# Kernel optimization log

Measured on AMD Instinct MI355X. Metric: run time of the kernel, lower is better.

The kernel has to match this reference:

```python
import jax, jax.numpy as jnp
import numpy as np

B, INSIZE, H, OUT, STEPS = 8192, 256, 128, 1, 50


def setup_inputs() -> dict:
    key = jax.random.key(0)
    ks = jax.random.split(key, 16)
    s = 0.05
    inp = {
        "x": jax.random.normal(ks[0], (B, INSIZE), jnp.float32),
        # encoder MLP: 256 -> 128 -> 128 -> 128 (ReLU on hiddens, linear out)
        "ew0": jax.random.normal(ks[1], (INSIZE, 128), jnp.float32) * s,
        "eb0": jnp.zeros((128,), jnp.float32),
        "ew1": jax.random.normal(ks[2], (128, 128), jnp.float32) * s,
        "eb1": jnp.zeros((128,), jnp.float32),
        "ew2": jax.random.normal(ks[3], (128, H), jnp.float32) * s,
        "eb2": jnp.zeros((H,), jnp.float32),
        # GRU (input size OUT=1, hidden H=128), PyTorch layout [3H, in]/[3H, H]
        "w_ih": jax.random.normal(ks[4], (3 * H, OUT), jnp.float32) * s,
        "w_hh": jax.random.normal(ks[5], (3 * H, H), jnp.float32) * s,
        "b_ih": jnp.zeros((3 * H,), jnp.float32),
        "b_hh": jnp.zeros((3 * H,), jnp.float32),
        # decoder MLP: 128 -> 16 -> 1
        "dw0": jax.random.normal(ks[6], (H, 16), jnp.float32) * s,
        "db0": jnp.zeros((16,), jnp.float32),
        "dw1": jax.random.normal(ks[7], (16, OUT), jnp.float32) * s,
        "db1": jnp.zeros((OUT,), jnp.float32),
    }
    return inp


def _gru_cell(x_t, h, w_ih, w_hh, b_ih, b_hh):
    # PyTorch GRU cell: gates ordered [r, z, n]
    gx = x_t @ w_ih.T + b_ih  # [B, 3H]
    gh = h @ w_hh.T + b_hh    # [B, 3H]
    r = jax.nn.sigmoid(gx[:, :H] + gh[:, :H])
    z = jax.nn.sigmoid(gx[:, H:2 * H] + gh[:, H:2 * H])
    n = jnp.tanh(gx[:, 2 * H:] + r * gh[:, 2 * H:])
    return (1.0 - z) * n + z * h


def reference(x, ew0, eb0, ew1, eb1, ew2, eb2, w_ih, w_hh, b_ih, b_hh, dw0, db0, dw1, db1):
    # encoder MLP -> initial hidden state
    h = jax.nn.relu(x @ ew0 + eb0)
    h = jax.nn.relu(h @ ew1 + eb1)
    h = h @ ew2 + eb2  # [B, H]

    def step(carry, _):
        prev, hc = carry
        hn = _gru_cell(prev, hc, w_ih, w_hh, b_ih, b_hh)
        d = jax.nn.relu(hn @ dw0 + db0)
        out = d @ dw1 + db1  # [B, 1]
        return (out, hn), out

    prev0 = jnp.zeros((x.shape[0], OUT), x.dtype)
    _, outs = jax.lax.scan(step, (prev0, h), None, length=STEPS)  # [50, B, 1]
    outs = jnp.squeeze(outs, -1).T  # [B, 50]
    # torch: cat([zeros, out_0..out_49], dim=1)[..., :-1] -> [zeros, out_0..out_48]
    zeros = jnp.zeros((x.shape[0], 1), x.dtype)
    return jnp.concatenate([zeros, outs], axis=1)[:, :-1]
```

## Files before the change

### kernel.cpp

```cpp
#include <hip/hip_runtime.h>

#define NTH 256

typedef _Float16 half8 __attribute__((ext_vector_type(8)));
typedef _Float16 half4 __attribute__((ext_vector_type(4)));
typedef __attribute__((ext_vector_type(4))) float floatx4;

#define LOG2E 1.44269504088896340736f

template<int CTRL>
__device__ __forceinline__ float dpp_add(float v) {
    int o = __builtin_amdgcn_update_dpp(0, __float_as_int(v), CTRL, 0xF, 0xF, true);
    return v + __int_as_float(o);
}

#define MFMA16 __builtin_amdgcn_mfma_f32_16x16x32_f16

template<int KTILES, int CMASK, int ROWH>
__device__ __forceinline__ void enc_layer(const _Float16* __restrict__ src,
                                          const float* __restrict__ W,
                                          const float* __restrict__ bias,
                                          int w, int quad, int l15,
                                          floatx4 acc[2]) {
    half8 bw[2][KTILES];
    #pragma unroll
    for (int nt = 0; nt < 2; nt++) {
        const int jc = w * 32 + nt * 16 + l15;
        #pragma unroll
        for (int kt = 0; kt < KTILES; kt++) {
            const int kb = kt * 32 + quad * 8;
            half8 hv;
            #pragma unroll
            for (int e = 0; e < 8; e++) hv[e] = (_Float16)W[(kb + e) * 128 + jc];
            bw[nt][kt] = hv;
        }
        const float bv = bias[jc];
        acc[nt] = (floatx4){bv, bv, bv, bv};
    }
    #pragma unroll
    for (int kt = 0; kt < KTILES; kt++) {
        const half8 av = *(const half8*)(src + l15 * ROWH +
                                         (((kt * 4 + quad) + l15) & CMASK) * 8);
        acc[0] = MFMA16(av, bw[0][kt], acc[0], 0, 0, 0);
        acc[1] = MFMA16(av, bw[1][kt], acc[1], 0, 0, 0);
    }
}

__device__ __forceinline__ void enc_store(_Float16* __restrict__ dst,
                                          const floatx4 acc[2],
                                          int w, int quad, int l15, bool relu) {
    #pragma unroll
    for (int nt = 0; nt < 2; nt++) {
        const int jc = w * 32 + nt * 16 + l15;
        #pragma unroll
        for (int reg = 0; reg < 4; reg++) {
            const int row = quad * 4 + reg;
            float v = acc[nt][reg];
            if (relu) v = fmaxf(v, 0.f);
            dst[row * 128 + ((((jc >> 3) + row) & 15) << 3) + (jc & 7)] = (_Float16)v;
        }
    }
}

__global__ __launch_bounds__(NTH, 2)
void gru_fused_kernel(const float* __restrict__ x,
                      const float* __restrict__ ew0, const float* __restrict__ eb0,
                      const float* __restrict__ ew1, const float* __restrict__ eb1,
                      const float* __restrict__ ew2, const float* __restrict__ eb2,
                      const float* __restrict__ w_ih, const float* __restrict__ w_hh,
                      const float* __restrict__ b_ih, const float* __restrict__ b_hh,
                      const float* __restrict__ dw0, const float* __restrict__ db0,
                      const float* __restrict__ dw1, const float* __restrict__ db1,
                      float* __restrict__ out) {
    __shared__ __align__(16) _Float16 encx[16 * 256];
    __shared__ __align__(16) _Float16 h1b[16 * 128];
    __shared__ __align__(16) _Float16 h16[2 * 16 * 128];
    __shared__ float outb[16][52];

    const int tid  = threadIdx.x;
    const int b0   = blockIdx.x * 16;
    const int lane = tid & 63;
    const int w    = tid >> 6;
    const int quad = lane >> 4;
    const int l15  = lane & 15;

    #pragma unroll
    for (int i = 0; i < 4; i++) {
        const int e = tid + i * NTH;
        const int row = e >> 6, c4 = e & 63;
        const float4 xv = *(const float4*)(x + (size_t)(b0 + row) * 256 + c4 * 4);
        half4 hv = {(_Float16)xv.x, (_Float16)xv.y, (_Float16)xv.z, (_Float16)xv.w};
        *(half4*)(encx + row * 256 + (((c4 >> 1) + row) & 31) * 8 + (c4 & 1) * 4) = hv;
    }
    __syncthreads();

    floatx4 ea[2];
    enc_layer<8, 31, 256>(encx, ew0, eb0, w, quad, l15, ea);
    enc_store(h1b, ea, w, quad, l15, true);
    __syncthreads();
    enc_layer<4, 15, 128>(h1b, ew1, eb1, w, quad, l15, ea);
    enc_store(encx, ea, w, quad, l15, true);
    __syncthreads();
    enc_layer<4, 15, 128>(encx, ew2, eb2, w, quad, l15, ea);
    float hold[2][4];
    #pragma unroll
    for (int nt = 0; nt < 2; nt++)
        #pragma unroll
        for (int reg = 0; reg < 4; reg++) hold[nt][reg] = ea[nt][reg];
    enc_store(h16, ea, w, quad, l15, false);
    if (tid < 16) outb[tid][0] = 0.f;

    half8 wb16[3][2][4];
    #pragma unroll
    for (int g = 0; g < 3; g++) {
        const float scale = (g == 2) ? 2.f * LOG2E : LOG2E;
        #pragma unroll
        for (int nt = 0; nt < 2; nt++) {
            const float* wrow = w_hh + (g * 128 + w * 32 + nt * 16 + l15) * 128;
            #pragma unroll
            for (int kt = 0; kt < 4; kt++) {
                const int kb = kt * 32 + quad * 8;
                half8 hv;
                #pragma unroll
                for (int e = 0; e < 8; e++) hv[e] = (_Float16)(wrow[kb + e] * scale);
                wb16[g][nt][kt] = hv;
            }
        }
    }
    half8 dw16[4];
    #pragma unroll
    for (int kt = 0; kt < 4; kt++) {
        half8 hv;
        #pragma unroll
        for (int e = 0; e < 8; e++)
            hv[e] = (_Float16)dw0[(kt * 32 + quad * 8 + e) * 16 + l15];
        dw16[kt] = hv;
    }
    float wr[2], wz[2], wn[2], c_r[2], c_z[2], c_n[2], bnih[2];
    int jcw[2];
    #pragma unroll
    for (int nt = 0; nt < 2; nt++) {
        const int jc = w * 32 + nt * 16 + l15;
        jcw[nt]  = jc;
        wr[nt]   = w_ih[jc] * LOG2E;
        wz[nt]   = w_ih[128 + jc] * LOG2E;
        wn[nt]   = w_ih[256 + jc] * (2.f * LOG2E);
        c_r[nt]  = (b_ih[jc] + b_hh[jc]) * LOG2E;
        c_z[nt]  = (b_ih[128 + jc] + b_hh[128 + jc]) * LOG2E;
        c_n[nt]  = b_hh[256 + jc] * (2.f * LOG2E);
        bnih[nt] = b_ih[256 + jc] * (2.f * LOG2E);
    }
    const float db0r = db0[l15];
    const float dw1r = dw1[l15];
    const float db1r = db1[0];
    __syncthreads();

    for (int t = 0; t <= 49; t++) {
        const int cur = t & 1, nxt = cur ^ 1;
        const _Float16* __restrict__ hc = h16 + cur * 2048;
        _Float16* __restrict__ hw = h16 + nxt * 2048;

        half8 ah[4];
        #pragma unroll
        for (int kt = 0; kt < 4; kt++)
            ah[kt] = *(const half8*)(hc + l15 * 128 +
                                     (((kt * 4 + quad) + l15) & 15) * 8);

        floatx4 dacc = (floatx4){0.f, 0.f, 0.f, 0.f};
        #pragma unroll
        for (int kt = 0; kt < 4; kt++)
            dacc = MFMA16(ah[kt], dw16[kt], dacc, 0, 0, 0);

        floatx4 acc[3][2];
        #pragma unroll
        for (int nt = 0; nt < 2; nt++) {
            acc[0][nt] = (floatx4){c_r[nt], c_r[nt], c_r[nt], c_r[nt]};
            acc[1][nt] = (floatx4){c_z[nt], c_z[nt], c_z[nt], c_z[nt]};
            acc[2][nt] = (floatx4){c_n[nt], c_n[nt], c_n[nt], c_n[nt]};
        }
        #pragma unroll
        for (int kt = 0; kt < 4; kt++)
            #pragma unroll
            for (int g = 0; g < 3; g++) {
                acc[g][0] = MFMA16(ah[kt], wb16[g][0][kt], acc[g][0], 0, 0, 0);
                acc[g][1] = MFMA16(ah[kt], wb16[g][1][kt], acc[g][1], 0, 0, 0);
            }

        float xp[4];
        #pragma unroll
        for (int reg = 0; reg < 4; reg++) {
            float v = fmaxf(dacc[reg] + db0r, 0.f) * dw1r;
            v = dpp_add<0x140>(v);
            v = dpp_add<0x141>(v);
            v = dpp_add<0x4E>(v);
            v = dpp_add<0xB1>(v);
            xp[reg] = (t == 0) ? 0.f : (v + db1r);
        }
        if (t > 0 && w == 0 && l15 == 0) {
            #pragma unroll
            for (int reg = 0; reg < 4; reg++)
                outb[quad * 4 + reg][t] = xp[reg];
        }

        if (t < 49) {
            #pragma unroll
            for (int nt = 0; nt < 2; nt++)
                #pragma unroll
                for (int reg = 0; reg < 4; reg++) {
                    const int row = quad * 4 + reg;
                    const float xpv = xp[reg];
                    const float hv0 = hold[nt][reg];
                    float gr = fmaf(xpv, wr[nt], acc[0][nt][reg]);
                    float gz = fmaf(xpv, wz[nt], acc[1][nt][reg]);
                    float Er = __builtin_amdgcn_exp2f(-gr);
                    float rg = __builtin_amdgcn_rcpf(1.f + Er);
                    float ys = fmaf(rg, acc[2][nt][reg], fmaf(xpv, wn[nt], bnih[nt]));
                    float Ey = __builtin_amdgcn_exp2f(ys);
                    float Ez = __builtin_amdgcn_exp2f(-gz);
                    float num = fmaf(Ez, Ey, -Ez) + fmaf(hv0, Ey, hv0);
                    float den = fmaf(Ey, Ez, Ey) + (Ez + 1.f);
                    const float hn = num * __builtin_amdgcn_rcpf(den);
                    hold[nt][reg] = hn;
                    hw[row * 128 + ((((jcw[nt] >> 3) + row) & 15) << 3) +
                       (jcw[nt] & 7)] = (_Float16)hn;
                }
        }
        __syncthreads();
    }

    for (int e = tid; e < 16 * 50; e += NTH) {
        const int b = e / 50;
        const int tcol = e - b * 50;
        out[(size_t)b0 * 50 + e] = outb[b][tcol];
    }
}

extern "C" void kernel_launch(void* const* d_in, const int* in_sizes, int n_in,
                              void* d_out, int out_size, void* d_ws, size_t ws_size,
                              hipStream_t stream) {
    const float* x   = (const float*)d_in[0];
    const float* ew0 = (const float*)d_in[1];
    const float* eb0 = (const float*)d_in[2];
    const float* ew1 = (const float*)d_in[3];
    const float* eb1 = (const float*)d_in[4];
    const float* ew2 = (const float*)d_in[5];
    const float* eb2 = (const float*)d_in[6];
    const float* wih = (const float*)d_in[7];
    const float* whh = (const float*)d_in[8];
    const float* bih = (const float*)d_in[9];
    const float* bhh = (const float*)d_in[10];
    const float* dw0 = (const float*)d_in[11];
    const float* db0 = (const float*)d_in[12];
    const float* dw1 = (const float*)d_in[13];
    const float* db1 = (const float*)d_in[14];
    float* out = (float*)d_out;

    gru_fused_kernel<<<512, NTH, 0, stream>>>(
        x, ew0, eb0, ew1, eb1, ew2, eb2, wih, whh, bih, bhh,
        dw0, db0, dw1, db1, out);
}
```

Before: 160.5 us.

## Permute hidden-state K layout for packed half2 stores and split decoder MFMA chain

```diff
diff --git a/kernel.cpp b/kernel.cpp
--- a/kernel.cpp
+++ b/kernel.cpp
@@ -4,6 +4,7 @@
 
 typedef _Float16 half8 __attribute__((ext_vector_type(8)));
 typedef _Float16 half4 __attribute__((ext_vector_type(4)));
+typedef _Float16 half2f __attribute__((ext_vector_type(2)));
 typedef __attribute__((ext_vector_type(4))) float floatx4;
 
 #define LOG2E 1.44269504088896340736f
@@ -15,6 +16,11 @@
 }
 
 #define MFMA16 __builtin_amdgcn_mfma_f32_16x16x32_f16
+
+__device__ __forceinline__ int kperm(int p) {
+    const int blk = p & ~31, q = p & 31;
+    return blk + ((q & 1) << 4) + (q >> 1);
+}
 
 template<int KTILES, int CMASK, int ROWH>
 __device__ __forceinline__ void enc_layer(const _Float16* __restrict__ src,
@@ -107,7 +113,14 @@
     for (int nt = 0; nt < 2; nt++)
         #pragma unroll
         for (int reg = 0; reg < 4; reg++) hold[nt][reg] = ea[nt][reg];
-    enc_store(h16, ea, w, quad, l15, false);
+    const int w4l = w * 4 + (l15 >> 2);
+    const int wo2 = (l15 & 3) * 2;
+    #pragma unroll
+    for (int reg = 0; reg < 4; reg++) {
+        const int row = quad * 4 + reg;
+        half2f hp = {(_Float16)ea[0][reg], (_Float16)ea[1][reg]};
+        *(half2f*)(h16 + row * 128 + (((w4l + row) & 15) << 3) + wo2) = hp;
+    }
     if (tid < 16) outb[tid][0] = 0.f;
 
     half8 wb16[3][2][4];
@@ -119,10 +132,12 @@
             const float* wrow = w_hh + (g * 128 + w * 32 + nt * 16 + l15) * 128;
             #pragma unroll
             for (int kt = 0; kt < 4; kt++) {
-                const int kb = kt * 32 + quad * 8;
                 half8 hv;
                 #pragma unroll
-                for (int e = 0; e < 8; e++) hv[e] = (_Float16)(wrow[kb + e] * scale);
+                for (int e = 0; e < 8; e++) {
+                    const int k = kperm(kt * 32 + quad * 8 + e);
+                    hv[e] = (_Float16)(wrow[k] * scale);
+                }
                 wb16[g][nt][kt] = hv;
             }
         }
@@ -132,16 +147,16 @@
     for (int kt = 0; kt < 4; kt++) {
         half8 hv;
         #pragma unroll
-        for (int e = 0; e < 8; e++)
-            hv[e] = (_Float16)dw0[(kt * 32 + quad * 8 + e) * 16 + l15];
+        for (int e = 0; e < 8; e++) {
+            const int k = kperm(kt * 32 + quad * 8 + e);
+            hv[e] = (_Float16)dw0[k * 16 + l15];
+        }
         dw16[kt] = hv;
     }
     float wr[2], wz[2], wn[2], c_r[2], c_z[2], c_n[2], bnih[2];
-    int jcw[2];
     #pragma unroll
     for (int nt = 0; nt < 2; nt++) {
         const int jc = w * 32 + nt * 16 + l15;
-        jcw[nt]  = jc;
         wr[nt]   = w_ih[jc] * LOG2E;
         wz[nt]   = w_ih[128 + jc] * LOG2E;
         wn[nt]   = w_ih[256 + jc] * (2.f * LOG2E);
@@ -155,6 +170,8 @@
     const float db1r = db1[0];
     __syncthreads();
 
+    if (blockIdx.x & 1) __builtin_amdgcn_s_sleep(13);
+
     for (int t = 0; t <= 49; t++) {
         const int cur = t & 1, nxt = cur ^ 1;
         const _Float16* __restrict__ hc = h16 + cur * 2048;
@@ -166,10 +183,12 @@
             ah[kt] = *(const half8*)(hc + l15 * 128 +
                                      (((kt * 4 + quad) + l15) & 15) * 8);
 
-        floatx4 dacc = (floatx4){0.f, 0.f, 0.f, 0.f};
-        #pragma unroll
-        for (int kt = 0; kt < 4; kt++)
-            dacc = MFMA16(ah[kt], dw16[kt], dacc, 0, 0, 0);
+        floatx4 dacc0 = (floatx4){db0r, db0r, db0r, db0r};
+        floatx4 dacc1 = (floatx4){0.f, 0.f, 0.f, 0.f};
+        dacc0 = MFMA16(ah[0], dw16[0], dacc0, 0, 0, 0);
+        dacc1 = MFMA16(ah[1], dw16[1], dacc1, 0, 0, 0);
+        dacc0 = MFMA16(ah[2], dw16[2], dacc0, 0, 0, 0);
+        dacc1 = MFMA16(ah[3], dw16[3], dacc1, 0, 0, 0);
 
         floatx4 acc[3][2];
         #pragma unroll
@@ -189,7 +208,7 @@
         float xp[4];
         #pragma unroll
         for (int reg = 0; reg < 4; reg++) {
-            float v = fmaxf(dacc[reg] + db0r, 0.f) * dw1r;
+            float v = fmaxf(dacc0[reg] + dacc1[reg], 0.f) * dw1r;
             v = dpp_add<0x140>(v);
             v = dpp_add<0x141>(v);
             v = dpp_add<0x4E>(v);
@@ -204,11 +223,12 @@
 
         if (t < 49) {
             #pragma unroll
-            for (int nt = 0; nt < 2; nt++)
+            for (int reg = 0; reg < 4; reg++) {
+                const int row = quad * 4 + reg;
+                const float xpv = xp[reg];
+                half2f hp;
                 #pragma unroll
-                for (int reg = 0; reg < 4; reg++) {
-                    const int row = quad * 4 + reg;
-                    const float xpv = xp[reg];
+                for (int nt = 0; nt < 2; nt++) {
                     const float hv0 = hold[nt][reg];
                     float gr = fmaf(xpv, wr[nt], acc[0][nt][reg]);
                     float gz = fmaf(xpv, wz[nt], acc[1][nt][reg]);
@@ -217,13 +237,16 @@
                     float ys = fmaf(rg, acc[2][nt][reg], fmaf(xpv, wn[nt], bnih[nt]));
                     float Ey = __builtin_amdgcn_exp2f(ys);
                     float Ez = __builtin_amdgcn_exp2f(-gz);
-                    float num = fmaf(Ez, Ey, -Ez) + fmaf(hv0, Ey, hv0);
-                    float den = fmaf(Ey, Ez, Ey) + (Ez + 1.f);
+                    float u   = Ey + 1.f;
+                    float t1  = fmaf(Ez, Ey, -Ez);
+                    float num = fmaf(hv0, u, t1);
+                    float den = fmaf(Ez, u, u);
                     const float hn = num * __builtin_amdgcn_rcpf(den);
                     hold[nt][reg] = hn;
-                    hw[row * 128 + ((((jcw[nt] >> 3) + row) & 15) << 3) +
-                       (jcw[nt] & 7)] = (_Float16)hn;
+                    hp[nt] = (_Float16)hn;
                 }
+                *(half2f*)(hw + row * 128 + (((w4l + row) & 15) << 3) + wo2) = hp;
+            }
         }
         __syncthreads();
     }
```

Measured after the change: 163.9 us. 1.02x slower.

## Double threads per block so each wave owns one 16-column tile

Applied to the files above, without the earlier changes.

```diff
diff --git a/kernel.cpp b/kernel.cpp
--- a/kernel.cpp
+++ b/kernel.cpp
@@ -1,6 +1,6 @@
 #include <hip/hip_runtime.h>
 
-#define NTH 256
+#define NTH 512
 
 typedef _Float16 half8 __attribute__((ext_vector_type(8)));
 typedef _Float16 half4 __attribute__((ext_vector_type(4)));
@@ -20,49 +20,40 @@
 __device__ __forceinline__ void enc_layer(const _Float16* __restrict__ src,
                                           const float* __restrict__ W,
                                           const float* __restrict__ bias,
-                                          int w, int quad, int l15,
-                                          floatx4 acc[2]) {
-    half8 bw[2][KTILES];
-    #pragma unroll
-    for (int nt = 0; nt < 2; nt++) {
-        const int jc = w * 32 + nt * 16 + l15;
-        #pragma unroll
-        for (int kt = 0; kt < KTILES; kt++) {
-            const int kb = kt * 32 + quad * 8;
-            half8 hv;
-            #pragma unroll
-            for (int e = 0; e < 8; e++) hv[e] = (_Float16)W[(kb + e) * 128 + jc];
-            bw[nt][kt] = hv;
-        }
-        const float bv = bias[jc];
-        acc[nt] = (floatx4){bv, bv, bv, bv};
-    }
+                                          int jc, int quad, int l15,
+                                          floatx4& acc) {
+    half8 bw[KTILES];
+    #pragma unroll
+    for (int kt = 0; kt < KTILES; kt++) {
+        const int kb = kt * 32 + quad * 8;
+        half8 hv;
+        #pragma unroll
+        for (int e = 0; e < 8; e++) hv[e] = (_Float16)W[(kb + e) * 128 + jc];
+        bw[kt] = hv;
+    }
+    const float bv = bias[jc];
+    acc = (floatx4){bv, bv, bv, bv};
     #pragma unroll
     for (int kt = 0; kt < KTILES; kt++) {
         const half8 av = *(const half8*)(src + l15 * ROWH +
                                          (((kt * 4 + quad) + l15) & CMASK) * 8);
-        acc[0] = MFMA16(av, bw[0][kt], acc[0], 0, 0, 0);
-        acc[1] = MFMA16(av, bw[1][kt], acc[1], 0, 0, 0);
+        acc = MFMA16(av, bw[kt], acc, 0, 0, 0);
     }
 }
 
 __device__ __forceinline__ void enc_store(_Float16* __restrict__ dst,
-                                          const floatx4 acc[2],
-                                          int w, int quad, int l15, bool relu) {
-    #pragma unroll
-    for (int nt = 0; nt < 2; nt++) {
-        const int jc = w * 32 + nt * 16 + l15;
-        #pragma unroll
-        for (int reg = 0; reg < 4; reg++) {
-            const int row = quad * 4 + reg;
-            float v = acc[nt][reg];
-            if (relu) v = fmaxf(v, 0.f);
-            dst[row * 128 + ((((jc >> 3) + row) & 15) << 3) + (jc & 7)] = (_Float16)v;
-        }
-    }
-}
-
-__global__ __launch_bounds__(NTH, 2)
+                                          const floatx4& acc,
+                                          int jc, int quad, int l15, bool relu) {
+    #pragma unroll
+    for (int reg = 0; reg < 4; reg++) {
+        const int row = quad * 4 + reg;
+        float v = acc[reg];
+        if (relu) v = fmaxf(v, 0.f);
+        dst[row * 128 + ((((jc >> 3) + row) & 15) << 3) + (jc & 7)] = (_Float16)v;
+    }
+}
+
+__global__ __launch_bounds__(NTH, 4)
 void gru_fused_kernel(const float* __restrict__ x,
                       const float* __restrict__ ew0, const float* __restrict__ eb0,
                       const float* __restrict__ ew1, const float* __restrict__ eb1,
@@ -75,6 +66,7 @@
     __shared__ __align__(16) _Float16 encx[16 * 256];
     __shared__ __align__(16) _Float16 h1b[16 * 128];
     __shared__ __align__(16) _Float16 h16[2 * 16 * 128];
+    __shared__ __align__(16) _Float16 dwT[16 * 128];
     __shared__ float outb[16][52];
 
     const int tid  = threadIdx.x;
@@ -83,73 +75,58 @@
     const int w    = tid >> 6;
     const int quad = lane >> 4;
     const int l15  = lane & 15;
-
-    #pragma unroll
-    for (int i = 0; i < 4; i++) {
+    const int jc   = w * 16 + l15;
+
+    #pragma unroll
+    for (int i = 0; i < 2; i++) {
         const int e = tid + i * NTH;
         const int row = e >> 6, c4 = e & 63;
         const float4 xv = *(const float4*)(x + (size_t)(b0 + row) * 256 + c4 * 4);
         half4 hv = {(_Float16)xv.x, (_Float16)xv.y, (_Float16)xv.z, (_Float16)xv.w};
         *(half4*)(encx + row * 256 + (((c4 >> 1) + row) & 31) * 8 + (c4 & 1) * 4) = hv;
     }
-    __syncthreads();
-
-    floatx4 ea[2];
-    enc_layer<8, 31, 256>(encx, ew0, eb0, w, quad, l15, ea);
-    enc_store(h1b, ea, w, quad, l15, true);
-    __syncthreads();
-    enc_layer<4, 15, 128>(h1b, ew1, eb1, w, quad, l15, ea);
-    enc_store(encx, ea, w, quad, l15, true);
-    __syncthreads();
-    enc_layer<4, 15, 128>(encx, ew2, eb2, w, quad, l15, ea);
-    float hold[2][4];
-    #pragma unroll
-    for (int nt = 0; nt < 2; nt++)
-        #pragma unroll
-        for (int reg = 0; reg < 4; reg++) hold[nt][reg] = ea[nt][reg];
-    enc_store(h16, ea, w, quad, l15, false);
+    for (int i = tid; i < 16 * 128; i += NTH) {
+        const int c = i & 15, k = i >> 4;
+        dwT[c * 128 + ((((k >> 3) + c) & 15) << 3) + (k & 7)] =
+            (_Float16)dw0[k * 16 + c];
+    }
+    __syncthreads();
+
+    floatx4 ea;
+    enc_layer<8, 31, 256>(encx, ew0, eb0, jc, quad, l15, ea);
+    enc_store(h1b, ea, jc, quad, l15, true);
+    __syncthreads();
+    enc_layer<4, 15, 128>(h1b, ew1, eb1, jc, quad, l15, ea);
+    enc_store(encx, ea, jc, quad, l15, true);
+    __syncthreads();
+    enc_layer<4, 15, 128>(encx, ew2, eb2, jc, quad, l15, ea);
+    float hold[4];
+    #pragma unroll
+    for (int reg = 0; reg < 4; reg++) hold[reg] = ea[reg];
+    enc_store(h16, ea, jc, quad, l15, false);
     if (tid < 16) outb[tid][0] = 0.f;
 
-    half8 wb16[3][2][4];
+    half8 wb16[3][4];
     #pragma unroll
     for (int g = 0; g < 3; g++) {
         const float scale = (g == 2) ? 2.f * LOG2E : LOG2E;
-        #pragma unroll
-        for (int nt = 0; nt < 2; nt++) {
-            const float* wrow = w_hh + (g * 128 + w * 32 + nt * 16 + l15) * 128;
-            #pragma unroll
-            for (int kt = 0; kt < 4; kt++) {
-                const int kb = kt * 32 + quad * 8;
-                half8 hv;
-                #pragma unroll
-                for (int e = 0; e < 8; e++) hv[e] = (_Float16)(wrow[kb + e] * scale);
-                wb16[g][nt][kt] = hv;
-            }
-        }
-    }
-    half8 dw16[4];
-    #pragma unroll
-    for (int kt = 0; kt < 4; kt++) {
-        half8 hv;
-        #pragma unroll
-        for (int e = 0; e < 8; e++)
-            hv[e] = (_Float16)dw0[(kt * 32 + quad * 8 + e) * 16 + l15];
-        dw16[kt] = hv;
-    }
-    float wr[2], wz[2], wn[2], c_r[2], c_z[2], c_n[2], bnih[2];
-    int jcw[2];
-    #pragma unroll
-    for (int nt = 0; nt < 2; nt++) {
-        const int jc = w * 32 + nt * 16 + l15;
-        jcw[nt]  = jc;
-        wr[nt]   = w_ih[jc] * LOG2E;
-        wz[nt]   = w_ih[128 + jc] * LOG2E;
-        wn[nt]   = w_ih[256 + jc] * (2.f * LOG2E);
-        c_r[nt]  = (b_ih[jc] + b_hh[jc]) * LOG2E;
-        c_z[nt]  = (b_ih[128 + jc] + b_hh[128 + jc]) * LOG2E;
-        c_n[nt]  = b_hh[256 + jc] * (2.f * LOG2E);
-        bnih[nt] = b_ih[256 + jc] * (2.f * LOG2E);
-    }
+        const float* wrow = w_hh + (g * 128 + jc) * 128;
+        #pragma unroll
+        for (int kt = 0; kt < 4; kt++) {
+            const int kb = kt * 32 + quad * 8;
+            half8 hv;
+            #pragma unroll
+            for (int e = 0; e < 8; e++) hv[e] = (_Float16)(wrow[kb + e] * scale);
+            wb16[g][kt] = hv;
+        }
+    }
+    const float wr   = w_ih[jc] * LOG2E;
+    const float wz   = w_ih[128 + jc] * LOG2E;
+    const float wn   = w_ih[256 + jc] * (2.f * LOG2E);
+    const float c_r  = (b_ih[jc] + b_hh[jc]) * LOG2E;
+    const float c_z  = (b_ih[128 + jc] + b_hh[128 + jc]) * LOG2E;
+    const float c_n  = b_hh[256 + jc] * (2.f * LOG2E);
+    const float bnih = b_ih[256 + jc] * (2.f * LOG2E);
     const float db0r = db0[l15];
     const float dw1r = dw1[l15];
     const float db1r = db1[0];
@@ -166,30 +143,30 @@
             ah[kt] = *(const half8*)(hc + l15 * 128 +
                                      (((kt * 4 + quad) + l15) & 15) * 8);
 
-        floatx4 dacc = (floatx4){0.f, 0.f, 0.f, 0.f};
+        floatx4 dacc0 = (floatx4){db0r, db0r, db0r, db0r};
+        floatx4 dacc1 = (floatx4){0.f, 0.f, 0.f, 0.f};
+        #pragma unroll
+        for (int kt = 0; kt < 4; kt++) {
+            const half8 dwk = *(const half8*)(dwT + l15 * 128 +
+                                              (((kt * 4 + quad) + l15) & 15) * 8);
+            if (kt & 1) dacc1 = MFMA16(ah[kt], dwk, dacc1, 0, 0, 0);
+            else        dacc0 = MFMA16(ah[kt], dwk, dacc0, 0, 0, 0);
+        }
+
+        floatx4 acc[3];
+        acc[0] = (floatx4){c_r, c_r, c_r, c_r};
+        acc[1] = (floatx4){c_z, c_z, c_z, c_z};
+        acc[2] = (floatx4){c_n, c_n, c_n, c_n};
         #pragma unroll
         for (int kt = 0; kt < 4; kt++)
-            dacc = MFMA16(ah[kt], dw16[kt], dacc, 0, 0, 0);
-
-        floatx4 acc[3][2];
-        #pragma unroll
-        for (int nt = 0; nt < 2; nt++) {
-            acc[0][nt] = (floatx4){c_r[nt], c_r[nt], c_r[nt], c_r[nt]};
-            acc[1][nt] = (floatx4){c_z[nt], c_z[nt], c_z[nt], c_z[nt]};
-            acc[2][nt] = (floatx4){c_n[nt], c_n[nt], c_n[nt], c_n[nt]};
-        }
-        #pragma unroll
-        for (int kt = 0; kt < 4; kt++)
-            #pragma unroll
-            for (int g = 0; g < 3; g++) {
-                acc[g][0] = MFMA16(ah[kt], wb16[g][0][kt], acc[g][0], 0, 0, 0);
-                acc[g][1] = MFMA16(ah[kt], wb16[g][1][kt], acc[g][1], 0, 0, 0);
-            }
+            #pragma unroll
+            for (int g = 0; g < 3; g++)
+                acc[g] = MFMA16(ah[kt], wb16[g][kt], acc[g], 0, 0, 0);
 
         float xp[4];
         #pragma unroll
         for (int reg = 0; reg < 4; reg++) {
-            float v = fmaxf(dacc[reg] + db0r, 0.f) * dw1r;
+            float v = fmaxf(dacc0[reg] + dacc1[reg], 0.f) * dw1r;
             v = dpp_add<0x140>(v);
             v = dpp_add<0x141>(v);
             v = dpp_add<0x4E>(v);
@@ -204,26 +181,26 @@
 
         if (t < 49) {
             #pragma unroll
-            for (int nt = 0; nt < 2; nt++)
-                #pragma unroll
-                for (int reg = 0; reg < 4; reg++) {
-                    const int row = quad * 4 + reg;
-                    const float xpv = xp[reg];
-                    const float hv0 = hold[nt][reg];
-                    float gr = fmaf(xpv, wr[nt], acc[0][nt][reg]);
-                    float gz = fmaf(xpv, wz[nt], acc[1][nt][reg]);
-                    float Er = __builtin_amdgcn_exp2f(-gr);
-                    float rg = __builtin_amdgcn_rcpf(1.f + Er);
-                    float ys = fmaf(rg, acc[2][nt][reg], fmaf(xpv, wn[nt], bnih[nt]));
-                    float Ey = __builtin_amdgcn_exp2f(ys);
-                    float Ez = __builtin_amdgcn_exp2f(-gz);
-                    float num = fmaf(Ez, Ey, -Ez) + fmaf(hv0, Ey, hv0);
-                    float den = fmaf(Ey, Ez, Ey) + (Ez + 1.f);
-                    const float hn = num * __builtin_amdgcn_rcpf(den);
-                    hold[nt][reg] = hn;
-                    hw[row * 128 + ((((jcw[nt] >> 3) + row) & 15) << 3) +
-                       (jcw[nt] & 7)] = (_Float16)hn;
-                }
+            for (int reg = 0; reg < 4; reg++) {
+                const int row = quad * 4 + reg;
+                const float xpv = xp[reg];
+                const float hv0 = hold[reg];
+                float gr = fmaf(xpv, wr, acc[0][reg]);
+                float gz = fmaf(xpv, wz, acc[1][reg]);
+                float Er = __builtin_amdgcn_exp2f(-gr);
+                float rg = __builtin_amdgcn_rcpf(1.f + Er);
+                float ys = fmaf(rg, acc[2][reg], fmaf(xpv, wn, bnih));
+                float Ey = __builtin_amdgcn_exp2f(ys);
+                float Ez = __builtin_amdgcn_exp2f(-gz);
+                float u   = Ey + 1.f;
+                float t1  = fmaf(Ez, Ey, -Ez);
+                float num = fmaf(hv0, u, t1);
+                float den = fmaf(Ez, u, u);
+                const float hn = num * __builtin_amdgcn_rcpf(den);
+                hold[reg] = hn;
+                hw[row * 128 + ((((jc >> 3) + row) & 15) << 3) + (jc & 7)] =
+                    (_Float16)hn;
+            }
         }
         __syncthreads();
     }
```

Result: slower. 171.8 us (+7.1%).
